# Kernel tuning notes

Measured on AMD Instinct MI355X. Metric: run time of the kernel, lower is better.

The kernel has to match this reference:

```python
import jax, jax.numpy as jnp
import numpy as np

NUM_EXPERTS = 8
HIDDEN = 1024
INTER = 2048
TOKENS = 2048
TOP_K = 2


def setup_inputs() -> dict:
    key = jax.random.key(0)
    k1, k2, k3, k4, k5 = jax.random.split(key, 5)
    hidden_states = jax.random.normal(k1, (TOKENS, HIDDEN), dtype=jnp.float32)
    top_k_index = jax.random.randint(k2, (TOKENS, TOP_K), 0, NUM_EXPERTS, dtype=jnp.int64)
    top_k_weights = jax.random.uniform(k3, (TOKENS, TOP_K), dtype=jnp.float32)
    # parameters, scaled like typical init
    gate_up_proj = jax.random.normal(k4, (NUM_EXPERTS, 2 * INTER, HIDDEN), dtype=jnp.float32) * (HIDDEN ** -0.5)
    down_proj = jax.random.normal(k5, (NUM_EXPERTS, HIDDEN, INTER), dtype=jnp.float32) * (INTER ** -0.5)
    return {
        "hidden_states": hidden_states,
        "top_k_index": top_k_index,
        "top_k_weights": top_k_weights,
        "gate_up_proj": gate_up_proj,
        "down_proj": down_proj,
    }


def reference(hidden_states, top_k_index, top_k_weights, gate_up_proj, down_proj):
    # combine weights per (token, expert): w[t, e] = sum_k 1[idx[t,k]==e] * tw[t,k]
    one_hot = jax.nn.one_hot(top_k_index, NUM_EXPERTS, dtype=hidden_states.dtype)  # [T, K, E]
    combine = jnp.einsum("tke,tk->te", one_hot, top_k_weights)  # [T, E]

    out = jnp.zeros_like(hidden_states)
    # fixed small loop over experts (structural, not a data dim)
    for e in range(NUM_EXPERTS):
        gu = hidden_states @ gate_up_proj[e].T  # [T, 2I]
        gate, up = jnp.split(gu, 2, axis=-1)
        h = jax.nn.gelu(gate, approximate=True) * up  # gelu_pytorch_tanh
        y = h @ down_proj[e].T  # [T, H]
        out = out + y * combine[:, e][:, None]
    return out
```

## Files before the change

kernel.cpp:

```cpp
#include <hip/hip_runtime.h>
#include <stdint.h>

#define T_TOK  2048
#define HID    1024
#define INTERN 2048
#define NEXP   8
#define MAXPOS 5248

typedef __attribute__((ext_vector_type(8))) short          bf16x8;
typedef __attribute__((ext_vector_type(4))) float          f32x4;
typedef __attribute__((ext_vector_type(8))) unsigned short u16x8;
typedef __attribute__((ext_vector_type(4))) unsigned short u16x4;

__device__ __forceinline__ unsigned short f32_to_bf16(float f) {
  unsigned int u = __float_as_uint(f);
  unsigned int r = (u + 0x7FFFu + ((u >> 16) & 1u)) >> 16;
  return (unsigned short)r;
}

__device__ __forceinline__ float bf16_to_f32(unsigned short h) {
  unsigned int u = ((unsigned int)h) << 16;
  return __uint_as_float(u);
}

__device__ __forceinline__ void gload_lds16(const void* g, void* l) {
  __builtin_amdgcn_global_load_lds(
      (const __attribute__((address_space(1))) unsigned int*)g,
      (__attribute__((address_space(3))) unsigned int*)l, 16, 0, 0);
}

__device__ __forceinline__ u16x8 cvt8(float4 a, float4 b) {
  u16x8 w;
  w[0] = f32_to_bf16(a.x); w[1] = f32_to_bf16(a.y);
  w[2] = f32_to_bf16(a.z); w[3] = f32_to_bf16(a.w);
  w[4] = f32_to_bf16(b.x); w[5] = f32_to_bf16(b.y);
  w[6] = f32_to_bf16(b.z); w[7] = f32_to_bf16(b.w);
  return w;
}

#define WAIT_VM0()    asm volatile("s_waitcnt vmcnt(0)" ::: "memory")
#define WAIT_VM4()    asm volatile("s_waitcnt vmcnt(4)" ::: "memory")
#define WAIT_LGKM0()  asm volatile("s_waitcnt lgkmcnt(0)" ::: "memory")
#define SCHED_FENCE() __builtin_amdgcn_sched_barrier(0)

__global__ void route_kernel(const int* __restrict__ tki,
                             const float* __restrict__ tkw,
                             int* __restrict__ counts,
                             int* __restrict__ offsets,
                             int* __restrict__ tok_list,
                             float* __restrict__ w_list,
                             int* __restrict__ pos_map,
                             float* __restrict__ wgt_map) {
  __shared__ int scnt[NEXP];
  __shared__ int soff[NEXP];
  int tid = threadIdx.x;
  if (tid < NEXP) scnt[tid] = 0;
  __syncthreads();
  for (int t = tid; t < T_TOK; t += 256) {
    int e0 = tki[2 * t] & 7;
    int e1 = tki[2 * t + 1] & 7;
    float w0 = tkw[2 * t];
    float w1 = tkw[2 * t + 1];
    if (e0 == e1) {
      int p = atomicAdd(&scnt[e0], 1);
      tok_list[e0 * T_TOK + p] = t;
      w_list [e0 * T_TOK + p] = w0 + w1;
      pos_map[2 * t]     = (p << 3) | e0;
      wgt_map[2 * t]     = w0 + w1;
      pos_map[2 * t + 1] = -1;
      wgt_map[2 * t + 1] = 0.0f;
    } else {
      int p = atomicAdd(&scnt[e0], 1);
      tok_list[e0 * T_TOK + p] = t;
      w_list [e0 * T_TOK + p] = w0;
      pos_map[2 * t]     = (p << 3) | e0;
      wgt_map[2 * t]     = w0;
      int q = atomicAdd(&scnt[e1], 1);
      tok_list[e1 * T_TOK + q] = t;
      w_list [e1 * T_TOK + q] = w1;
      pos_map[2 * t + 1] = (q << 3) | e1;
      wgt_map[2 * t + 1] = w1;
    }
  }
  __syncthreads();
  if (tid == 0) {
    int acc = 0;
    for (int e = 0; e < NEXP; ++e) {
      counts[e]  = scnt[e];
      offsets[e] = acc;
      soff[e]    = acc;
      acc += ((scnt[e] + 127) >> 7) << 7;
    }
  }
  __syncthreads();
  for (int i = tid; i < 2 * T_TOK; i += 256) {
    int v = pos_map[i];
    if (v >= 0) pos_map[i] = soff[v & 7] + (v >> 3);
  }
}

__global__ void cvt_x_kernel(const float* __restrict__ x, unsigned short* __restrict__ xb) {
  int i = blockIdx.x * 256 + threadIdx.x;
  float4 v = ((const float4*)x)[i];
  u16x4 o;
  o[0] = f32_to_bf16(v.x); o[1] = f32_to_bf16(v.y);
  o[2] = f32_to_bf16(v.z); o[3] = f32_to_bf16(v.w);
  *((u16x4*)(xb + 4 * (size_t)i)) = o;
}

#define G1_STEP(CUR, NXT, TILE, CG0, CG1, CU0, CU1, LG0, LG1, LU0, LU1)                            \
  {                                                                                                \
    WAIT_VM4(); SCHED_FENCE();                                                                     \
    __builtin_amdgcn_s_barrier(); SCHED_FENCE();                                                   \
    {                                                                                              \
      int ka_ = ((TILE) + 1) * 32; if (ka_ >= HID) ka_ = 0;                                        \
      char* base_ = (char*)&As[NXT][0][0][0];                                                      \
      gload_lds16(asrc + ka_ + akg * 8,       base_ + (size_t)tid * 16);                           \
      gload_lds16(asrc + ka_ + (akg + 2) * 8, base_ + 4096 + (size_t)tid * 16);                    \
    }                                                                                              \
    SCHED_FENCE();                                                                                 \
    {                                                                                              \
      int kb_ = ((TILE) + 2) * 32; if (kb_ >= HID) kb_ = 0;                                        \
      const float4* gp_ = (const float4*)(gsrc + kb_);                                             \
      const float4* up_ = (const float4*)(usrc + kb_);                                             \
      LG0 = gp_[0]; LG1 = gp_[1]; LU0 = up_[0]; LU1 = up_[1];                                      \
    }                                                                                              \
    SCHED_FENCE();                                                                                 \
    {                                                                                              \
      int kg_ = lane >> 4;                                                                         \
      int rl_ = lane & 15;                                                                         \
      bf16x8 af[4], gf[2], uf[2];                                                                  \
      for (int m = 0; m < 4; ++m)                                                                  \
        af[m] = *((const bf16x8*)&As[CUR][kg_][wm * 64 + m * 16 + rl_][0]);                        \
      for (int n = 0; n < 2; ++n) {                                                                \
        int r_ = (wn * 32 + n * 16 + rl_) ^ kg_;                                                   \
        gf[n] = *((const bf16x8*)&Gs[CUR][kg_][r_][0]);                                            \
        uf[n] = *((const bf16x8*)&Us[CUR][kg_][r_][0]);                                            \
      }                                                                                            \
      for (int m = 0; m < 4; ++m)                                                                  \
        for (int n = 0; n < 2; ++n) {                                                              \
          accg[m][n] = __builtin_amdgcn_mfma_f32_16x16x32_bf16(af[m], gf[n], accg[m][n], 0, 0, 0); \
          accu[m][n] = __builtin_amdgcn_mfma_f32_16x16x32_bf16(af[m], uf[n], accu[m][n], 0, 0, 0); \
        }                                                                                          \
    }                                                                                              \
    *((u16x8*)&Gs[NXT][bq][brw][0]) = cvt8(CG0, CG1);                                              \
    *((u16x8*)&Us[NXT][bq][brw][0]) = cvt8(CU0, CU1);                                              \
    WAIT_LGKM0(); SCHED_FENCE();                                                                   \
  }

__global__ __launch_bounds__(256, 3)
void gemm1_kernel(const unsigned short* __restrict__ xb,
                  const float* __restrict__ gup,
                  const int* __restrict__ counts,
                  const int* __restrict__ offsets,
                  const int* __restrict__ tok_list,
                  unsigned short* __restrict__ hbuf) {
  int lid = blockIdx.x;
  int xcd = lid & 7;
  int k2  = lid >> 3;
  int ne  = xcd * 32 + (k2 >> 4);
  int mq  = k2 & 15;
  int nb  = ne & 31;
  int e   = ne >> 5;

  int Ne = counts[e];
  int m0 = mq * 128;
  if (m0 >= Ne) return;
  int n0  = nb * 64;
  int off = offsets[e];

  __shared__ __align__(16) unsigned short As[2][4][128][8];
  __shared__ __align__(16) unsigned short Gs[2][4][64][8];
  __shared__ __align__(16) unsigned short Us[2][4][64][8];

  int tid  = threadIdx.x;
  int lane = tid & 63;
  int wave = tid >> 6;
  int wm = wave >> 1;
  int wn = wave & 1;

  int arow = tid & 127;
  int akg  = tid >> 7;
  int rg   = m0 + arow;
  int tok  = (rg < Ne) ? tok_list[e * T_TOK + rg] : 0;
  const unsigned short* asrc = xb + (size_t)tok * HID;

  int brow = tid >> 2;
  int bq   = tid & 3;
  const float* gsrc = gup + (size_t)e * (2 * INTERN) * HID + (size_t)(n0 + brow) * HID + bq * 8;
  const float* usrc = gsrc + (size_t)INTERN * HID;
  int brw = brow ^ bq;

  f32x4 accg[4][2], accu[4][2];
#pragma unroll
  for (int m = 0; m < 4; ++m)
#pragma unroll
    for (int n = 0; n < 2; ++n) {
      accg[m][n] = (f32x4){0.f, 0.f, 0.f, 0.f};
      accu[m][n] = (f32x4){0.f, 0.f, 0.f, 0.f};
    }

  float4 xg0, xg1, xu0, xu1;
  float4 yg0, yg1, yu0, yu1;

  {
    char* base = (char*)&As[0][0][0][0];
    gload_lds16(asrc + akg * 8,       base + (size_t)tid * 16);
    gload_lds16(asrc + (akg + 2) * 8, base + 4096 + (size_t)tid * 16);
    const float4* gp = (const float4*)gsrc;
    const float4* up = (const float4*)usrc;
    float4 tg0 = gp[0], tg1 = gp[1], tu0 = up[0], tu1 = up[1];
    *((u16x8*)&Gs[0][bq][brw][0]) = cvt8(tg0, tg1);
    *((u16x8*)&Us[0][bq][brw][0]) = cvt8(tu0, tu1);
    const float4* gp1 = (const float4*)(gsrc + 32);
    const float4* up1 = (const float4*)(usrc + 32);
    yg0 = gp1[0]; yg1 = gp1[1]; yu0 = up1[0]; yu1 = up1[1];
    WAIT_LGKM0(); SCHED_FENCE();
  }

  const int NT = HID / 32;
  for (int tt = 0; tt < NT; tt += 2) {
    G1_STEP(0, 1, tt,     yg0, yg1, yu0, yu1,  xg0, xg1, xu0, xu1);
    G1_STEP(1, 0, tt + 1, xg0, xg1, xu0, xu1,  yg0, yg1, yu0, yu1);
  }
  WAIT_VM0();

  int rl = lane & 15;
  int rq = lane >> 4;
  size_t hb_base = (size_t)((off + m0) >> 7) * (INTERN * 128);
#pragma unroll
  for (int m = 0; m < 4; ++m) {
#pragma unroll
    for (int n = 0; n < 2; ++n) {
      int col = n0 + wn * 32 + n * 16 + rl;
      size_t cbase = hb_base + (size_t)(col >> 3) * 1024 + (col & 7);
#pragma unroll
      for (int j = 0; j < 4; ++j) {
        int lr = wm * 64 + m * 16 + rq * 4 + j;
        if (m0 + lr < Ne) {
          float gv = accg[m][n][j];
          float uv = accu[m][n][j];
          float tt2 = gv + 0.044715f * gv * gv * gv;
          float a  = gv / (1.0f + __expf(-1.5957691216f * tt2));
          hbuf[cbase + (size_t)lr * 8] = f32_to_bf16(a * uv);
        }
      }
    }
  }
}

#define G2_STEP(CUR, NXT, TILE, CB0, CB1, CB2, CB3, LB0, LB1, LB2, LB3)                            \
  {                                                                                                \
    WAIT_VM4(); SCHED_FENCE();                                                                     \
    __builtin_amdgcn_s_barrier(); SCHED_FENCE();                                                   \
    {                                                                                              \
      int ka_ = ((TILE) + 1) * 64; if (ka_ >= INTERN) ka_ = 0;                                     \
      char* base_ = (char*)&As[NXT][0][0][0];                                                      \
      const unsigned short* ak_ = asrc + (size_t)ka_ * 128;                                        \
      for (int o = 0; o < 4; ++o)                                                                  \
        gload_lds16(ak_ + o * 2048 + (size_t)tid * 8, base_ + o * 4096 + (size_t)tid * 16);        \
    }                                                                                              \
    SCHED_FENCE();                                                                                 \
    {                                                                                              \
      int kb_ = ((TILE) + 2) * 64; if (kb_ >= INTERN) kb_ = 0;                                     \
      const float4* bp_ = (const float4*)(bsrc + kb_);                                             \
      LB0 = bp_[0]; LB1 = bp_[1]; LB2 = bp_[2]; LB3 = bp_[3];                                      \
    }                                                                                              \
    SCHED_FENCE();                                                                                 \
    for (int kk = 0; kk < 2; ++kk) {                                                               \
      int kg_ = kk * 4 + (lane >> 4);                                                              \
      int rl_ = lane & 15;                                                                         \
      bf16x8 af[4], bfv[2];                                                                        \
      for (int m = 0; m < 4; ++m)                                                                  \
        af[m] = *((const bf16x8*)&As[CUR][kg_][wm * 64 + m * 16 + rl_][0]);                        \
      for (int n = 0; n < 2; ++n)                                                                  \
        bfv[n] = *((const bf16x8*)&Bs[CUR][kg_][(wn * 32 + n * 16 + rl_) ^ kg_][0]);               \
      for (int m = 0; m < 4; ++m)                                                                  \
        for (int n = 0; n < 2; ++n)                                                                \
          acc[m][n] = __builtin_amdgcn_mfma_f32_16x16x32_bf16(af[m], bfv[n], acc[m][n], 0, 0, 0);  \
    }                                                                                              \
    *((u16x8*)&Bs[NXT][kgw0][brow ^ kgw0][0]) = cvt8(CB0, CB1);                                    \
    *((u16x8*)&Bs[NXT][kgw1][brow ^ kgw1][0]) = cvt8(CB2, CB3);                                    \
    WAIT_LGKM0(); SCHED_FENCE();                                                                   \
  }

__global__ __launch_bounds__(256, 2)
void gemm2_kernel(const unsigned short* __restrict__ hbuf,
                  const float* __restrict__ down,
                  const int* __restrict__ counts,
                  const int* __restrict__ offsets,
                  unsigned short* __restrict__ ybuf) {
  int lid = blockIdx.x;
  int xcd = lid & 7;
  int k2  = lid >> 3;
  int ne  = xcd * 16 + (k2 >> 4);
  int mq  = k2 & 15;
  int nb  = ne & 15;
  int e   = ne >> 4;

  int Ne = counts[e];
  int m0 = mq * 128;
  if (m0 >= Ne) return;
  int n0  = nb * 64;
  int off = offsets[e];

  __shared__ __align__(16) unsigned short As[2][8][128][8];
  __shared__ __align__(16) unsigned short Bs[2][8][64][8];

  int tid  = threadIdx.x;
  int lane = tid & 63;
  int wave = tid >> 6;
  int wm = wave >> 1;
  int wn = wave & 1;

  const unsigned short* asrc = hbuf + (size_t)((off + m0) >> 7) * (INTERN * 128);

  int brow = tid >> 2;
  int bq   = tid & 3;
  int kgw0 = bq * 2, kgw1 = bq * 2 + 1;
  const float* bsrc = down + (size_t)e * HID * INTERN + (size_t)(n0 + brow) * INTERN + bq * 16;

  f32x4 acc[4][2];
#pragma unroll
  for (int m = 0; m < 4; ++m)
#pragma unroll
    for (int n = 0; n < 2; ++n) acc[m][n] = (f32x4){0.f, 0.f, 0.f, 0.f};

  float4 xb0, xb1, xb2, xb3;
  float4 yb0, yb1, yb2, yb3;

  {
    char* base = (char*)&As[0][0][0][0];
#pragma unroll
    for (int o = 0; o < 4; ++o)
      gload_lds16(asrc + o * 2048 + (size_t)tid * 8, base + o * 4096 + (size_t)tid * 16);
    const float4* bp = (const float4*)bsrc;
    float4 t0 = bp[0], t1 = bp[1], t2 = bp[2], t3 = bp[3];
    *((u16x8*)&Bs[0][kgw0][brow ^ kgw0][0]) = cvt8(t0, t1);
    *((u16x8*)&Bs[0][kgw1][brow ^ kgw1][0]) = cvt8(t2, t3);
    const float4* bp1 = (const float4*)(bsrc + 64);
    yb0 = bp1[0]; yb1 = bp1[1]; yb2 = bp1[2]; yb3 = bp1[3];
    WAIT_LGKM0(); SCHED_FENCE();
  }

  const int NT = INTERN / 64;
  for (int tt = 0; tt < NT; tt += 2) {
    G2_STEP(0, 1, tt,     yb0, yb1, yb2, yb3,  xb0, xb1, xb2, xb3);
    G2_STEP(1, 0, tt + 1, xb0, xb1, xb2, xb3,  yb0, yb1, yb2, yb3);
  }
  WAIT_VM0();

  int rl = lane & 15;
  int rq = lane >> 4;
#pragma unroll
  for (int m = 0; m < 4; ++m) {
#pragma unroll
    for (int n = 0; n < 2; ++n) {
      int col = n0 + wn * 32 + n * 16 + rl;
#pragma unroll
      for (int j = 0; j < 4; ++j) {
        int lr = wm * 64 + m * 16 + rq * 4 + j;
        if (m0 + lr < Ne)
          ybuf[(size_t)(off + m0 + lr) * HID + col] = f32_to_bf16(acc[m][n][j]);
      }
    }
  }
}

__global__ void combine_kernel(const int* __restrict__ pos_map,
                               const float* __restrict__ wgt_map,
                               const unsigned short* __restrict__ ybuf,
                               float* __restrict__ out) {
  int i  = blockIdx.x * 256 + threadIdx.x;
  int t  = i >> 7;
  int c8 = i & 127;
  int p0 = pos_map[2 * t];
  int p1 = pos_map[2 * t + 1];
  float w0 = wgt_map[2 * t];
  float w1 = wgt_map[2 * t + 1];
  float acc[8];
#pragma unroll
  for (int j = 0; j < 8; ++j) acc[j] = 0.f;
  if (p0 >= 0) {
    u16x8 v = *((const u16x8*)(ybuf + (size_t)p0 * HID + c8 * 8));
#pragma unroll
    for (int j = 0; j < 8; ++j) acc[j] += w0 * bf16_to_f32(v[j]);
  }
  if (p1 >= 0) {
    u16x8 v = *((const u16x8*)(ybuf + (size_t)p1 * HID + c8 * 8));
#pragma unroll
    for (int j = 0; j < 8; ++j) acc[j] += w1 * bf16_to_f32(v[j]);
  }
  float4 o0 = make_float4(acc[0], acc[1], acc[2], acc[3]);
  float4 o1 = make_float4(acc[4], acc[5], acc[6], acc[7]);
  float4* dst = (float4*)(out + (size_t)t * HID + c8 * 8);
  dst[0] = o0;
  dst[1] = o1;
}

extern "C" void kernel_launch(void* const* d_in, const int* in_sizes, int n_in,
                              void* d_out, int out_size, void* d_ws, size_t ws_size,
                              hipStream_t stream) {
  (void)in_sizes; (void)n_in; (void)out_size;
  const float* hidden = (const float*)d_in[0];
  const int*   tki    = (const int*)d_in[1];
  const float* tkw    = (const float*)d_in[2];
  const float* gup    = (const float*)d_in[3];
  const float* down   = (const float*)d_in[4];
  float* out = (float*)d_out;
  char*  ws  = (char*)d_ws;

  int*   counts   = (int*)  (ws + 0);
  int*   offsets  = (int*)  (ws + 64);
  int*   tok_list = (int*)  (ws + 256);
  int*   pos_map  = (int*)  (ws + 65792);
  float* wgt_map  = (float*)(ws + 82176);
  float* w_list   = (float*)(ws + 98560);
  unsigned short* xb   = (unsigned short*)(ws + 164096);
  unsigned short* hbuf = (unsigned short*)(ws + 4358400);
  unsigned short* ybuf = (unsigned short*)(ws + 25854208);

  if (ws_size < 36602112ull) return;

  hipLaunchKernelGGL(route_kernel, dim3(1), dim3(256), 0, stream,
                     tki, tkw, counts, offsets, tok_list, w_list, pos_map, wgt_map);
  hipLaunchKernelGGL(cvt_x_kernel, dim3((T_TOK * HID / 4) / 256), dim3(256), 0, stream,
                     hidden, xb);
  hipLaunchKernelGGL(gemm1_kernel, dim3(32 * 16 * NEXP), dim3(256), 0, stream,
                     xb, gup, counts, offsets, tok_list, hbuf);
  hipLaunchKernelGGL(gemm2_kernel, dim3(16 * 16 * NEXP), dim3(256), 0, stream,
                     hbuf, down, counts, offsets, ybuf);
  hipLaunchKernelGGL(combine_kernel, dim3(T_TOK * HID / 8 / 256), dim3(256), 0, stream,
                     pos_map, wgt_map, ybuf, out);
}
```

Baseline: 155.0 us.

## Use 3D grid mapping, raise MFMA wave priority, add prologue vmem wait

Both GEMM kernels drop the XCD-aware 1D block remapping in favor of a plain 3D grid (n-tile, m-tile, expert). The MFMA loops are wrapped in s_setprio(1)/s_setprio(0) to favor waves issuing matrix ops. An extra vmcnt(0) wait is added after the prologue so that async global-to-LDS loads finish before the main loop. Losing the XCD grouping may reduce L2 reuse of weight tiles across blocks on the same XCD, and the added wait serializes part of the prologue.

After: 166.6 us. +7.5%, slower.

```diff
diff --git a/kernel.cpp b/kernel.cpp
--- a/kernel.cpp
+++ b/kernel.cpp
@@ -137,11 +137,13 @@
         gf[n] = *((const bf16x8*)&Gs[CUR][kg_][r_][0]);                                            \
         uf[n] = *((const bf16x8*)&Us[CUR][kg_][r_][0]);                                            \
       }                                                                                            \
+      __builtin_amdgcn_s_setprio(1);                                                               \
       for (int m = 0; m < 4; ++m)                                                                  \
         for (int n = 0; n < 2; ++n) {                                                              \
           accg[m][n] = __builtin_amdgcn_mfma_f32_16x16x32_bf16(af[m], gf[n], accg[m][n], 0, 0, 0); \
           accu[m][n] = __builtin_amdgcn_mfma_f32_16x16x32_bf16(af[m], uf[n], accu[m][n], 0, 0, 0); \
         }                                                                                          \
+      __builtin_amdgcn_s_setprio(0);                                                               \
     }                                                                                              \
     *((u16x8*)&Gs[NXT][bq][brw][0]) = cvt8(CG0, CG1);                                              \
     *((u16x8*)&Us[NXT][bq][brw][0]) = cvt8(CU0, CU1);                                              \
@@ -155,18 +157,11 @@
                   const int* __restrict__ offsets,
                   const int* __restrict__ tok_list,
                   unsigned short* __restrict__ hbuf) {
-  int lid = blockIdx.x;
-  int xcd = lid & 7;
-  int k2  = lid >> 3;
-  int ne  = xcd * 32 + (k2 >> 4);
-  int mq  = k2 & 15;
-  int nb  = ne & 31;
-  int e   = ne >> 5;
-
+  int e  = blockIdx.z;
   int Ne = counts[e];
-  int m0 = mq * 128;
+  int m0 = blockIdx.y * 128;
   if (m0 >= Ne) return;
-  int n0  = nb * 64;
+  int n0  = blockIdx.x * 64;
   int off = offsets[e];
 
   __shared__ __align__(16) unsigned short As[2][4][128][8];
@@ -215,7 +210,9 @@
     const float4* gp1 = (const float4*)(gsrc + 32);
     const float4* up1 = (const float4*)(usrc + 32);
     yg0 = gp1[0]; yg1 = gp1[1]; yu0 = up1[0]; yu1 = up1[1];
-    WAIT_LGKM0(); SCHED_FENCE();
+    WAIT_LGKM0();
+    WAIT_VM0();
+    SCHED_FENCE();
   }
 
   const int NT = HID / 32;
@@ -275,9 +272,11 @@
         af[m] = *((const bf16x8*)&As[CUR][kg_][wm * 64 + m * 16 + rl_][0]);                        \
       for (int n = 0; n < 2; ++n)                                                                  \
         bfv[n] = *((const bf16x8*)&Bs[CUR][kg_][(wn * 32 + n * 16 + rl_) ^ kg_][0]);               \
+      __builtin_amdgcn_s_setprio(1);                                                               \
       for (int m = 0; m < 4; ++m)                                                                  \
         for (int n = 0; n < 2; ++n)                                                                \
           acc[m][n] = __builtin_amdgcn_mfma_f32_16x16x32_bf16(af[m], bfv[n], acc[m][n], 0, 0, 0);  \
+      __builtin_amdgcn_s_setprio(0);                                                               \
     }                                                                                              \
     *((u16x8*)&Bs[NXT][kgw0][brow ^ kgw0][0]) = cvt8(CB0, CB1);                                    \
     *((u16x8*)&Bs[NXT][kgw1][brow ^ kgw1][0]) = cvt8(CB2, CB3);                                    \
@@ -290,18 +289,11 @@
                   const int* __restrict__ counts,
                   const int* __restrict__ offsets,
                   unsigned short* __restrict__ ybuf) {
-  int lid = blockIdx.x;
-  int xcd = lid & 7;
-  int k2  = lid >> 3;
-  int ne  = xcd * 16 + (k2 >> 4);
-  int mq  = k2 & 15;
-  int nb  = ne & 15;
-  int e   = ne >> 4;
-
+  int e  = blockIdx.z;
   int Ne = counts[e];
-  int m0 = mq * 128;
+  int m0 = blockIdx.y * 128;
   if (m0 >= Ne) return;
-  int n0  = nb * 64;
+  int n0  = blockIdx.x * 64;
   int off = offsets[e];
 
   __shared__ __align__(16) unsigned short As[2][8][128][8];
@@ -340,7 +332,9 @@
     *((u16x8*)&Bs[0][kgw1][brow ^ kgw1][0]) = cvt8(t2, t3);
     const float4* bp1 = (const float4*)(bsrc + 64);
     yb0 = bp1[0]; yb1 = bp1[1]; yb2 = bp1[2]; yb3 = bp1[3];
-    WAIT_LGKM0(); SCHED_FENCE();
+    WAIT_LGKM0();
+    WAIT_VM0();
+    SCHED_FENCE();
   }
 
   const int NT = INTERN / 64;
@@ -426,9 +420,9 @@
                      tki, tkw, counts, offsets, tok_list, w_list, pos_map, wgt_map);
   hipLaunchKernelGGL(cvt_x_kernel, dim3((T_TOK * HID / 4) / 256), dim3(256), 0, stream,
                      hidden, xb);
-  hipLaunchKernelGGL(gemm1_kernel, dim3(32 * 16 * NEXP), dim3(256), 0, stream,
+  hipLaunchKernelGGL(gemm1_kernel, dim3(INTERN / 64, T_TOK / 128, NEXP), dim3(256), 0, stream,
                      xb, gup, counts, offsets, tok_list, hbuf);
-  hipLaunchKernelGGL(gemm2_kernel, dim3(16 * 16 * NEXP), dim3(256), 0, stream,
+  hipLaunchKernelGGL(gemm2_kernel, dim3(HID / 64, T_TOK / 128, NEXP), dim3(256), 0, stream,
                      hbuf, down, counts, offsets, ybuf);
   hipLaunchKernelGGL(combine_kernel, dim3(T_TOK * HID / 8 / 256), dim3(256), 0, stream,
                      pos_map, wgt_map, ybuf, out);
```
